# Optimization experiments

Hardware: AMD Instinct MI355X
Metric: run time of the kernel (lower is better)

Reference implementation:

```python
import jax, jax.numpy as jnp
import numpy as np

B, T, C = 4, 2048, 2048
H, D, L = 16, 128, 512


def _rope(x, cos, sin):
    # x: [B, T, H, D]; cos/sin: [T, D//2]; consecutive-pair complex rotation
    x2 = x.reshape(*x.shape[:-1], -1, 2)
    x0, x1 = x2[..., 0], x2[..., 1]
    c = cos[None, :, None, :]
    s = sin[None, :, None, :]
    o0 = x0 * c - x1 * s
    o1 = x0 * s + x1 * c
    return jnp.stack([o0, o1], axis=-1).reshape(x.shape)


def setup_inputs() -> dict:
    key = jax.random.key(0)
    ks = jax.random.split(key, 8)
    x = jax.random.normal(ks[0], (B, T, C), dtype=jnp.float32)
    # rotary table, theta = 10000
    inv_freq = 1.0 / (10000.0 ** (np.arange(0, D, 2, dtype=np.float32) / D))
    ang = np.outer(np.arange(T, dtype=np.float32), inv_freq)
    freqs_cos = jnp.asarray(np.cos(ang), dtype=jnp.float32)
    freqs_sin = jnp.asarray(np.sin(ang), dtype=jnp.float32)
    sc = 0.02
    wq = sc * jax.random.normal(ks[1], (H * D, C), dtype=jnp.float32)
    wkv_down = sc * jax.random.normal(ks[2], (L, C), dtype=jnp.float32)
    wk_up = sc * jax.random.normal(ks[3], (D, L), dtype=jnp.float32)
    wv_up = sc * jax.random.normal(ks[4], (D, L), dtype=jnp.float32)
    wo = sc * jax.random.normal(ks[5], (C, H * D), dtype=jnp.float32)
    return {"x": x, "freqs_cos": freqs_cos, "freqs_sin": freqs_sin,
            "wq": wq, "wkv_down": wkv_down, "wk_up": wk_up,
            "wv_up": wv_up, "wo": wo}


def reference(x, freqs_cos, freqs_sin, wq, wkv_down, wk_up, wv_up, wo):
    Bc, Tc, Cc = x.shape
    # query projection -> [B, T, H, D]
    q = jnp.einsum('btc,ec->bte', x, wq).reshape(Bc, Tc, H, D)
    # shared latent KV: [B, T, L]
    kv_latent = jnp.einsum('btc,lc->btl', x, wkv_down)
    # up-project to single shared head: [B, T, D]
    k = jnp.einsum('btl,dl->btd', kv_latent, wk_up)
    v = jnp.einsum('btl,dl->btd', kv_latent, wv_up)
    # RoPE on q (per head) and k (single shared head)
    q = _rope(q, freqs_cos, freqs_sin)
    k = _rope(k[:, :, None, :], freqs_cos, freqs_sin)[:, :, 0, :]
    # causal SDPA; k/v are shared across heads (MLA) so avoid expanding them
    scale = 1.0 / jnp.sqrt(jnp.asarray(D, dtype=x.dtype))
    scores = jnp.einsum('bthd,bsd->bhts', q, k) * scale  # [B, H, T, S]
    causal = jnp.tril(jnp.ones((Tc, Tc), dtype=bool))
    scores = jnp.where(causal[None, None, :, :], scores, jnp.finfo(x.dtype).min)
    probs = jax.nn.softmax(scores, axis=-1)
    y = jnp.einsum('bhts,bsd->bthd', probs, v).reshape(Bc, Tc, H * D)
    return jnp.einsum('bte,ce->btc', y, wo)
```

## Files before the change

### kernel.cpp

```cpp
#include <hip/hip_runtime.h>
#include <hip/hip_bf16.h>
#include <cstddef>

#define BB 4
#define TT 2048
#define CC 2048
#define HH 16
#define DD 128
#define LL 512

typedef _Float16 f16;
typedef f16 f16x2 __attribute__((ext_vector_type(2)));
typedef f16 f16x4 __attribute__((ext_vector_type(4)));
typedef f16 f16x8 __attribute__((ext_vector_type(8)));
typedef float f32x4 __attribute__((ext_vector_type(4)));

__device__ __forceinline__ void async_load16(void* lptr, const void* gptr) {
  __builtin_amdgcn_global_load_lds(
      (const __attribute__((address_space(1))) unsigned int*)gptr,
      (__attribute__((address_space(3))) unsigned int*)lptr, 16, 0, 0);
}

__global__ __launch_bounds__(512, 2) void mla_gemm_256(
    const f16* __restrict__ A, const f16* __restrict__ B,
    float* __restrict__ C, int M, int N, int K) {
  __shared__ __align__(16) f16 smem[2][2][256 * 64];

  const int tid = threadIdx.x;
  const int lane = tid & 63;
  const int w = tid >> 6;
  const int lnm = lane & 15, quad = lane >> 4;
  const int wm = w >> 2, wn = w & 3;

  const int nwg = gridDim.x;
  const int bid0 = blockIdx.x;
  const int q8 = nwg >> 3, r8 = nwg & 7;
  const int xcd = bid0 & 7, lid = bid0 >> 3;
  const int wg =
      (xcd < r8 ? xcd * (q8 + 1) : r8 * (q8 + 1) + (xcd - r8) * q8) + lid;
  const int ntc = N >> 8;
  const int m0 = (wg / ntc) * 256;
  const int n0 = (wg % ntc) * 256;

  const int srow = tid >> 3;
  const int sch = (tid & 7) ^ ((tid >> 3) & 7);
  const f16* Ag = A + (size_t)(m0 + srow) * K + sch * 8;
  const f16* Bg = B + (size_t)(n0 + srow) * K + sch * 8;

  auto stage = [&](int bi, int k0, int h) {
    const int mat = h >> 1;
    const int rb = (h & 1) * 128;
    const f16* g = (mat ? Bg : Ag) + (size_t)rb * K + k0;
    f16* l = &smem[bi][mat][rb * 64 + tid * 8];
    async_load16(l, g);
    async_load16(l + 4096, g + (size_t)64 * K);
  };

  const int rx8 = lnm & 7;
  auto rdA = [&](const f16* Ab, int i, int ks) -> f16x8 {
    return *(const f16x8*)&Ab[(wm * 128 + i * 16 + lnm) * 64 +
                              (((ks * 4 + quad) ^ rx8) * 8)];
  };
  auto rdB = [&](const f16* Bb, int j, int ks) -> f16x8 {
    return *(const f16x8*)&Bb[(wn * 64 + j * 16 + lnm) * 64 +
                              (((ks * 4 + quad) ^ rx8) * 8)];
  };

  f32x4 acc[8][4] = {};

  const int NT = K >> 6;

  stage(0, 0, 0);
  stage(0, 0, 1);
  stage(0, 0, 2);
  stage(0, 0, 3);
  stage(1, 64, 0);
  asm volatile("s_waitcnt vmcnt(2)" ::: "memory");
  __builtin_amdgcn_s_barrier();

  for (int t = 0; t < NT; ++t) {
    const int bi = t & 1;
    const f16* Ab = smem[bi][0];
    const f16* Bb = smem[bi][1];
    const int k1 = (t + 1 < NT ? t + 1 : t) << 6;
    const int k2 = (t + 2 < NT ? t + 2 : t) << 6;

    f16x8 Ar[4][2], Br[2][2];

#pragma unroll
    for (int i = 0; i < 4; i++)
#pragma unroll
      for (int ks = 0; ks < 2; ks++) Ar[i][ks] = rdA(Ab, i, ks);
#pragma unroll
    for (int j = 0; j < 2; j++)
#pragma unroll
      for (int ks = 0; ks < 2; ks++) Br[j][ks] = rdB(Bb, j, ks);
    stage(bi ^ 1, k1, 1);
    __builtin_amdgcn_s_barrier();
    asm volatile("s_waitcnt lgkmcnt(0)" ::: "memory");
    __builtin_amdgcn_s_setprio(1);
#pragma unroll
    for (int i = 0; i < 4; i++)
#pragma unroll
      for (int j = 0; j < 2; j++)
#pragma unroll
        for (int ks = 0; ks < 2; ks++)
          acc[i][j] = __builtin_amdgcn_mfma_f32_16x16x32_f16(
              Ar[i][ks], Br[j][ks], acc[i][j], 0, 0, 0);
    __builtin_amdgcn_s_setprio(0);
    __builtin_amdgcn_s_barrier();

#pragma unroll
    for (int j = 0; j < 2; j++)
#pragma unroll
      for (int ks = 0; ks < 2; ks++) Br[j][ks] = rdB(Bb, 2 + j, ks);
    stage(bi ^ 1, k1, 2);
    __builtin_amdgcn_s_barrier();
    asm volatile("s_waitcnt lgkmcnt(0)" ::: "memory");
    __builtin_amdgcn_s_setprio(1);
#pragma unroll
    for (int i = 0; i < 4; i++)
#pragma unroll
      for (int j = 0; j < 2; j++)
#pragma unroll
        for (int ks = 0; ks < 2; ks++)
          acc[i][2 + j] = __builtin_amdgcn_mfma_f32_16x16x32_f16(
              Ar[i][ks], Br[j][ks], acc[i][2 + j], 0, 0, 0);
    __builtin_amdgcn_s_setprio(0);
    __builtin_amdgcn_s_barrier();

#pragma unroll
    for (int i = 0; i < 4; i++)
#pragma unroll
      for (int ks = 0; ks < 2; ks++) Ar[i][ks] = rdA(Ab, 4 + i, ks);
    stage(bi ^ 1, k1, 3);
    __builtin_amdgcn_s_barrier();
    asm volatile("s_waitcnt lgkmcnt(0)" ::: "memory");
    __builtin_amdgcn_s_setprio(1);
#pragma unroll
    for (int i = 0; i < 4; i++)
#pragma unroll
      for (int j = 0; j < 2; j++)
#pragma unroll
        for (int ks = 0; ks < 2; ks++)
          acc[4 + i][2 + j] = __builtin_amdgcn_mfma_f32_16x16x32_f16(
              Ar[i][ks], Br[j][ks], acc[4 + i][2 + j], 0, 0, 0);
    __builtin_amdgcn_s_setprio(0);
    __builtin_amdgcn_s_barrier();

#pragma unroll
    for (int j = 0; j < 2; j++)
#pragma unroll
      for (int ks = 0; ks < 2; ks++) Br[j][ks] = rdB(Bb, j, ks);
    stage(bi, k2, 0);
    __builtin_amdgcn_s_barrier();
    asm volatile("s_waitcnt lgkmcnt(0)" ::: "memory");
    __builtin_amdgcn_s_setprio(1);
#pragma unroll
    for (int i = 0; i < 4; i++)
#pragma unroll
      for (int j = 0; j < 2; j++)
#pragma unroll
        for (int ks = 0; ks < 2; ks++)
          acc[4 + i][j] = __builtin_amdgcn_mfma_f32_16x16x32_f16(
              Ar[i][ks], Br[j][ks], acc[4 + i][j], 0, 0, 0);
    __builtin_amdgcn_s_setprio(0);
    asm volatile("s_waitcnt vmcnt(2)" ::: "memory");
    __builtin_amdgcn_s_barrier();
  }

  asm volatile("s_waitcnt vmcnt(0)" ::: "memory");

#pragma unroll
  for (int i = 0; i < 8; i++)
#pragma unroll
    for (int r = 0; r < 4; r++) {
      float* crow = C + (size_t)(m0 + wm * 128 + i * 16 + quad * 4 + r) * N +
                    n0 + wn * 64 + lnm;
#pragma unroll
      for (int j = 0; j < 4; j++) crow[j * 16] = acc[i][j][r];
    }
}

__global__ __launch_bounds__(256) void mla_gemm_mfma(
    const f16* __restrict__ A, const f16* __restrict__ B,
    float* __restrict__ C, int M, int N, int K) {
  __shared__ f16 As[128 * 32];
  __shared__ f16 Bs[128 * 32];

  const int tid = threadIdx.x;
  const int lane = tid & 63;
  const int w = tid >> 6;
  const int lnm = lane & 15, quad = lane >> 4;
  const int wm = w >> 1, wn = w & 1;
  const int m0 = blockIdx.y * 128;
  const int n0 = blockIdx.x * 128;

  const int srow = tid >> 2;
  const int skoff = (tid & 3) * 8;

  f32x4 acc[4][4] = {};

  for (int k0 = 0; k0 < K; k0 += 32) {
    const f16* ag = A + (size_t)(m0 + srow) * K + k0 + skoff;
    const f16* bg = B + (size_t)(n0 + srow) * K + k0 + skoff;
    async_load16(&As[(size_t)tid * 8], ag);
    async_load16(&As[(size_t)(256 + tid) * 8], ag + (size_t)64 * K);
    async_load16(&Bs[(size_t)tid * 8], bg);
    async_load16(&Bs[(size_t)(256 + tid) * 8], bg + (size_t)64 * K);
    __syncthreads();

    f16x8 af[4], bf[4];
#pragma unroll
    for (int i = 0; i < 4; i++)
      af[i] = *(const f16x8*)&As[(wm * 64 + i * 16 + lnm) * 32 + quad * 8];
#pragma unroll
    for (int j = 0; j < 4; j++)
      bf[j] = *(const f16x8*)&Bs[(wn * 64 + j * 16 + lnm) * 32 + quad * 8];
#pragma unroll
    for (int i = 0; i < 4; i++)
#pragma unroll
      for (int j = 0; j < 4; j++)
        acc[i][j] = __builtin_amdgcn_mfma_f32_16x16x32_f16(af[i], bf[j],
                                                           acc[i][j], 0, 0, 0);
    __syncthreads();
  }

#pragma unroll
  for (int i = 0; i < 4; i++)
#pragma unroll
    for (int r = 0; r < 4; r++) {
      float* crow = C + (size_t)(m0 + wm * 64 + i * 16 + quad * 4 + r) * N +
                    n0 + wn * 64 + lnm;
#pragma unroll
      for (int j = 0; j < 4; j++) crow[j * 16] = acc[i][j][r];
    }
}

__global__ __launch_bounds__(256) void mla_cvt_f16(
    const float4* __restrict__ in, f16* __restrict__ out, int n4) {
  int i = blockIdx.x * 256 + threadIdx.x;
  if (i >= n4) return;
  float4 v = in[i];
  f16x4 r = {(f16)v.x, (f16)v.y, (f16)v.z, (f16)v.w};
  *(f16x4*)(out + (size_t)i * 4) = r;
}

__global__ __launch_bounds__(256) void mla_rope_cvt(
    const float2* __restrict__ x, f16* __restrict__ o,
    const float* __restrict__ cosb, const float* __restrict__ sinb,
    int Hh, float scale, int total) {
  int idx = blockIdx.x * blockDim.x + threadIdx.x;
  if (idx >= total) return;
  const int Dh = DD / 2;
  int i = idx % Dh;
  int t = (idx / (Dh * Hh)) % TT;
  float c = cosb[t * Dh + i];
  float s = sinb[t * Dh + i];
  float2 v = x[idx];
  f16x2 r;
  r.x = (f16)((v.x * c - v.y * s) * scale);
  r.y = (f16)((v.x * s + v.y * c) * scale);
  *(f16x2*)(o + (size_t)idx * 2) = r;
}

__global__ __launch_bounds__(256) void mla_transpose_v(
    const float* __restrict__ v, f16* __restrict__ vt) {
  __shared__ float tl[32][33];
  const int b = blockIdx.z;
  const int t0 = blockIdx.x * 32;
  const int d0 = blockIdx.y * 32;
  const int tx = threadIdx.x & 31;
  const int ty = threadIdx.x >> 5;
#pragma unroll
  for (int k = 0; k < 4; k++)
    tl[ty + 8 * k][tx] = v[((size_t)(b * TT + t0 + ty + 8 * k)) * DD + d0 + tx];
  __syncthreads();
#pragma unroll
  for (int k = 0; k < 4; k++)
    vt[((size_t)(b * DD + d0 + ty + 8 * k)) * TT + t0 + tx] =
        (f16)tl[tx][ty + 8 * k];
}

__global__ __launch_bounds__(256, 2) void mla_flash2(
    const f16* __restrict__ qh, const f16* __restrict__ kh,
    const f16* __restrict__ vth, f16* __restrict__ y) {
  __shared__ f16 Ks[64 * 128];
  __shared__ f16 Vs[128 * 64];

  const int tid = threadIdx.x;
  const int lane = tid & 63;
  const int w = tid >> 6;
  const int lnm = lane & 15, quad = lane >> 4;

  const int bid = blockIdx.x;
  const int qt = (TT / 128 - 1) - (bid >> 6);
  const int bh = bid & 63;
  const int b = bh >> 4, h = bh & 15;
  const int q0b = qt * 128;
  const int q0 = q0b + w * 32;

  f16x8 qf[2][4];
#pragma unroll
  for (int qnb = 0; qnb < 2; qnb++) {
    const f16* qrow =
        qh + ((size_t)(b * TT + q0 + qnb * 16 + lnm) * HH + h) * DD;
#pragma unroll
    for (int c = 0; c < 4; c++)
      qf[qnb][c] = *(const f16x8*)(qrow + c * 32 + quad * 8);
  }

  f32x4 O[2][8] = {};
  float l_acc[2] = {0.f, 0.f};

  const int nst = (q0b + 128) / 64;
  const int wmax = q0 + 31;
  const f16* kbase = kh + (size_t)b * TT * DD;
  const f16* vbase = vth + (size_t)b * DD * TT;

  const int ks_row = tid >> 4;
  const int ks_col = ((tid & 15) ^ (tid >> 4)) * 8;
  const int vs_row = tid >> 3;
  const int vs_col = ((tid & 7) ^ ((tid >> 3) & 7)) * 8;

  for (int st = 0; st < nst; st++) {
    const int s0 = st * 64;
#pragma unroll
    for (int i = 0; i < 4; i++)
      async_load16(&Ks[(size_t)(i * 256 + tid) * 8],
                   kbase + (size_t)(s0 + i * 16 + ks_row) * DD + ks_col);
#pragma unroll
    for (int i = 0; i < 4; i++)
      async_load16(&Vs[(size_t)(i * 256 + tid) * 8],
                   vbase + (size_t)(i * 32 + vs_row) * TT + s0 + vs_col);
    __syncthreads();

    if (s0 <= wmax) {
      f32x4 S[2][4] = {};
#pragma unroll
      for (int sb = 0; sb < 4; sb++) {
        const int sl = sb * 16 + lnm;
#pragma unroll
        for (int c = 0; c < 4; c++) {
          f16x8 ka =
              *(const f16x8*)&Ks[sl * 128 + ((c * 4 + quad) ^ lnm) * 8];
          S[0][sb] = __builtin_amdgcn_mfma_f32_16x16x32_f16(ka, qf[0][c],
                                                            S[0][sb], 0, 0, 0);
          S[1][sb] = __builtin_amdgcn_mfma_f32_16x16x32_f16(ka, qf[1][c],
                                                            S[1][sb], 0, 0, 0);
        }
      }

      f16x4 P[2][4];
      const bool domask = (s0 + 63 > q0);
#pragma unroll
      for (int qnb = 0; qnb < 2; qnb++) {
        const int m_abs = q0 + qnb * 16 + lnm;
        float lp = 0.f;
#pragma unroll
        for (int sb = 0; sb < 4; sb++) {
          const int srow = s0 + sb * 16 + quad * 4;
          f16x4 ph;
#pragma unroll
          for (int j = 0; j < 4; j++) {
            float p = __expf(S[qnb][sb][j]);
            if (domask && (srow + j > m_abs)) p = 0.f;
            lp += p;
            ph[j] = (f16)p;
          }
          P[qnb][sb] = ph;
        }
        l_acc[qnb] += lp;
      }

#pragma unroll
      for (int sb = 0; sb < 4; sb++) {
        const int chb = sb * 2 + (quad >> 1);
        const int soff = (quad & 1) * 4;
#pragma unroll
        for (int db = 0; db < 8; db++) {
          const int d = db * 16 + lnm;
          f16x4 vb =
              *(const f16x4*)&Vs[d * 64 + ((chb ^ (d & 7)) * 8) + soff];
          O[0][db] = __builtin_amdgcn_mfma_f32_16x16x16f16(P[0][sb], vb,
                                                           O[0][db], 0, 0, 0);
          O[1][db] = __builtin_amdgcn_mfma_f32_16x16x16f16(P[1][sb], vb,
                                                           O[1][db], 0, 0, 0);
        }
      }
    }
    __syncthreads();
  }

#pragma unroll
  for (int qnb = 0; qnb < 2; qnb++) {
    float l = l_acc[qnb];
    l += __shfl_xor(l, 16, 64);
    l += __shfl_xor(l, 32, 64);
    l_acc[qnb] = l;
  }

#pragma unroll
  for (int qnb = 0; qnb < 2; qnb++) {
    float linv[4];
#pragma unroll
    for (int r = 0; r < 4; r++)
      linv[r] = 1.f / __shfl(l_acc[qnb], quad * 4 + r, 64);
#pragma unroll
    for (int db = 0; db < 8; db++)
#pragma unroll
      for (int r = 0; r < 4; r++) {
        size_t off =
            ((size_t)(b * TT + q0 + qnb * 16 + quad * 4 + r) * HH + h) * DD +
            db * 16 + lnm;
        y[off] = (f16)(O[qnb][db][r] * linv[r]);
      }
  }
}

extern "C" void kernel_launch(void* const* d_in, const int* in_sizes, int n_in,
                              void* d_out, int out_size, void* d_ws,
                              size_t ws_size, hipStream_t stream) {
  const float* x      = (const float*)d_in[0];
  const float* fcos   = (const float*)d_in[1];
  const float* fsin   = (const float*)d_in[2];
  const float* wq     = (const float*)d_in[3];
  const float* wdown  = (const float*)d_in[4];
  const float* wk_up  = (const float*)d_in[5];
  const float* wv_up  = (const float*)d_in[6];
  const float* wo     = (const float*)d_in[7];
  float* out = (float*)d_out;

  const int M = BB * TT;

  float* ws = (float*)d_ws;
  float* q      = ws;
  float* kv     = q + (size_t)M * CC;
  float* kk     = kv + (size_t)M * LL;
  float* vv     = kk + (size_t)M * DD;
  f16*   xh     = (f16*)(vv + (size_t)M * DD);
  f16*   wqh    = xh + (size_t)M * CC;
  f16*   wdownh = wqh + (size_t)CC * CC;
  f16*   wkuph  = wdownh + (size_t)LL * CC;
  f16*   wvuph  = wkuph + (size_t)DD * LL;
  f16*   woh    = wvuph + (size_t)DD * LL;
  f16*   kvh    = woh + (size_t)CC * CC;
  f16*   khb    = kvh + (size_t)M * LL;
  f16*   vth    = khb + (size_t)M * DD;
  f16*   qh     = xh;
  f16*   yh     = (f16*)q;

  dim3 blk(256);

  mla_cvt_f16<<<(M * CC / 4 + 255) / 256, blk, 0, stream>>>(
      (const float4*)x, xh, M * CC / 4);
  mla_cvt_f16<<<(CC * CC / 4 + 255) / 256, blk, 0, stream>>>(
      (const float4*)wq, wqh, CC * CC / 4);
  mla_cvt_f16<<<(LL * CC / 4 + 255) / 256, blk, 0, stream>>>(
      (const float4*)wdown, wdownh, LL * CC / 4);
  mla_cvt_f16<<<(DD * LL / 4 + 255) / 256, blk, 0, stream>>>(
      (const float4*)wk_up, wkuph, DD * LL / 4);
  mla_cvt_f16<<<(DD * LL / 4 + 255) / 256, blk, 0, stream>>>(
      (const float4*)wv_up, wvuph, DD * LL / 4);
  mla_cvt_f16<<<(CC * CC / 4 + 255) / 256, blk, 0, stream>>>(
      (const float4*)wo, woh, CC * CC / 4);

  mla_gemm_256<<<dim3((M / 256) * (CC / 256)), dim3(512), 0, stream>>>(
      xh, wqh, q, M, CC, CC);
  mla_gemm_mfma<<<dim3(LL / 128, M / 128), blk, 0, stream>>>(
      xh, wdownh, kv, M, LL, CC);

  mla_cvt_f16<<<(M * LL / 4 + 255) / 256, blk, 0, stream>>>(
      (const float4*)kv, kvh, M * LL / 4);
  mla_gemm_mfma<<<dim3(DD / 128, M / 128), blk, 0, stream>>>(
      kvh, wkuph, kk, M, DD, LL);
  mla_gemm_mfma<<<dim3(DD / 128, M / 128), blk, 0, stream>>>(
      kvh, wvuph, vv, M, DD, LL);

  {
    const float SCL = 0.08838834764831845f;
    int total_q = BB * TT * HH * (DD / 2);
    mla_rope_cvt<<<(total_q + 255) / 256, blk, 0, stream>>>(
        (const float2*)q, qh, fcos, fsin, HH, SCL, total_q);
    int total_k = BB * TT * (DD / 2);
    mla_rope_cvt<<<(total_k + 255) / 256, blk, 0, stream>>>(
        (const float2*)kk, khb, fcos, fsin, 1, 1.0f, total_k);
  }

  mla_transpose_v<<<dim3(TT / 32, DD / 32, BB), blk, 0, stream>>>(vv, vth);

  mla_flash2<<<dim3(BB * HH * (TT / 128)), blk, 0, stream>>>(qh, khb, vth, yh);

  mla_gemm_256<<<dim3((M / 256) * (CC / 256)), dim3(512), 0, stream>>>(
      yh, woh, out, M, CC, CC);
}
```

Measured before the change: 485.2 us.

## Fuse Q RoPE into GEMM epilogue and double-buffer flash attention K/V

The Q projection GEMM gains a templated epilogue that applies RoPE and the softmax scale, then writes fp16 directly. This removes the fp32 Q write and the separate rope/convert pass over the largest activation. The flash attention kernel double-buffers its K/V LDS tiles so the next tile's async loads overlap compute, and it switches the PV product to 16x16x32 MFMA with setprio hints. Costs are doubled LDS per block, which may reduce occupancy, and scattered per-element fp16 stores with cos/sin gathers in the epilogue. The workspace layout changes so qh and yh no longer alias xh.

```diff
diff --git a/kernel.cpp b/kernel.cpp
--- a/kernel.cpp
+++ b/kernel.cpp
@@ -21,9 +21,11 @@
       (__attribute__((address_space(3))) unsigned int*)lptr, 16, 0, 0);
 }
 
+template <int EPI>
 __global__ __launch_bounds__(512, 2) void mla_gemm_256(
     const f16* __restrict__ A, const f16* __restrict__ B,
-    float* __restrict__ C, int M, int N, int K) {
+    void* __restrict__ Cv, int M, int N, int K,
+    const float* __restrict__ cosb, const float* __restrict__ sinb) {
   __shared__ __align__(16) f16 smem[2][2][256 * 64];
 
   const int tid = threadIdx.x;
@@ -171,15 +173,40 @@
 
   asm volatile("s_waitcnt vmcnt(0)" ::: "memory");
 
-#pragma unroll
-  for (int i = 0; i < 8; i++)
-#pragma unroll
-    for (int r = 0; r < 4; r++) {
-      float* crow = C + (size_t)(m0 + wm * 128 + i * 16 + quad * 4 + r) * N +
-                    n0 + wn * 64 + lnm;
-#pragma unroll
-      for (int j = 0; j < 4; j++) crow[j * 16] = acc[i][j][r];
-    }
+  if constexpr (EPI == 0) {
+    float* C = (float*)Cv;
+#pragma unroll
+    for (int i = 0; i < 8; i++)
+#pragma unroll
+      for (int r = 0; r < 4; r++) {
+        float* crow = C + (size_t)(m0 + wm * 128 + i * 16 + quad * 4 + r) * N +
+                      n0 + wn * 64 + lnm;
+#pragma unroll
+        for (int j = 0; j < 4; j++) crow[j * 16] = acc[i][j][r];
+      }
+  } else {
+    f16* C = (f16*)Cv;
+    const float SCL = 0.08838834764831845f;
+#pragma unroll
+    for (int i = 0; i < 8; i++)
+#pragma unroll
+      for (int r = 0; r < 4; r++) {
+        const int m = m0 + wm * 128 + i * 16 + quad * 4 + r;
+        const int t = m & (TT - 1);
+#pragma unroll
+        for (int j = 0; j < 4; j++) {
+          const int col = n0 + wn * 64 + j * 16 + lnm;
+          float v = acc[i][j][r];
+          float u = __shfl_xor(v, 1, 64);
+          const int fi = (col & (DD - 1)) >> 1;
+          const float ct = cosb[t * (DD / 2) + fi];
+          const float st2 = sinb[t * (DD / 2) + fi];
+          const float o =
+              (lnm & 1) ? (u * st2 + v * ct) : (v * ct - u * st2);
+          C[(size_t)m * N + col] = (f16)(o * SCL);
+        }
+      }
+  }
 }
 
 __global__ __launch_bounds__(256) void mla_gemm_mfma(
@@ -285,8 +312,8 @@
 __global__ __launch_bounds__(256, 2) void mla_flash2(
     const f16* __restrict__ qh, const f16* __restrict__ kh,
     const f16* __restrict__ vth, f16* __restrict__ y) {
-  __shared__ f16 Ks[64 * 128];
-  __shared__ f16 Vs[128 * 64];
+  __shared__ f16 Ks[2][64 * 128];
+  __shared__ f16 Vs[2][128 * 64];
 
   const int tid = threadIdx.x;
   const int lane = tid & 63;
@@ -323,35 +350,48 @@
   const int vs_row = tid >> 3;
   const int vs_col = ((tid & 7) ^ ((tid >> 3) & 7)) * 8;
 
+  auto stage = [&](int buf, int st) {
+    const int s0 = st * 64;
+#pragma unroll
+    for (int i = 0; i < 4; i++)
+      async_load16(&Ks[buf][(size_t)(i * 256 + tid) * 8],
+                   kbase + (size_t)(s0 + i * 16 + ks_row) * DD + ks_col);
+#pragma unroll
+    for (int i = 0; i < 4; i++)
+      async_load16(&Vs[buf][(size_t)(i * 256 + tid) * 8],
+                   vbase + (size_t)(i * 32 + vs_row) * TT + s0 + vs_col);
+  };
+
+  stage(0, 0);
+  __syncthreads();
+
   for (int st = 0; st < nst; st++) {
+    const int cur = st & 1;
     const int s0 = st * 64;
-#pragma unroll
-    for (int i = 0; i < 4; i++)
-      async_load16(&Ks[(size_t)(i * 256 + tid) * 8],
-                   kbase + (size_t)(s0 + i * 16 + ks_row) * DD + ks_col);
-#pragma unroll
-    for (int i = 0; i < 4; i++)
-      async_load16(&Vs[(size_t)(i * 256 + tid) * 8],
-                   vbase + (size_t)(i * 32 + vs_row) * TT + s0 + vs_col);
-    __syncthreads();
+    if (st + 1 < nst) stage(cur ^ 1, st + 1);
 
     if (s0 <= wmax) {
+      const f16* Kc = Ks[cur];
+      const f16* Vc = Vs[cur];
+
       f32x4 S[2][4] = {};
+      __builtin_amdgcn_s_setprio(1);
 #pragma unroll
       for (int sb = 0; sb < 4; sb++) {
         const int sl = sb * 16 + lnm;
 #pragma unroll
         for (int c = 0; c < 4; c++) {
           f16x8 ka =
-              *(const f16x8*)&Ks[sl * 128 + ((c * 4 + quad) ^ lnm) * 8];
+              *(const f16x8*)&Kc[sl * 128 + ((c * 4 + quad) ^ lnm) * 8];
           S[0][sb] = __builtin_amdgcn_mfma_f32_16x16x32_f16(ka, qf[0][c],
                                                             S[0][sb], 0, 0, 0);
           S[1][sb] = __builtin_amdgcn_mfma_f32_16x16x32_f16(ka, qf[1][c],
                                                             S[1][sb], 0, 0, 0);
         }
       }
-
-      f16x4 P[2][4];
+      __builtin_amdgcn_s_setprio(0);
+
+      f16x8 P8[2][2];
       const bool domask = (s0 + 63 > q0);
 #pragma unroll
       for (int qnb = 0; qnb < 2; qnb++) {
@@ -360,34 +400,42 @@
 #pragma unroll
         for (int sb = 0; sb < 4; sb++) {
           const int srow = s0 + sb * 16 + quad * 4;
-          f16x4 ph;
 #pragma unroll
           for (int j = 0; j < 4; j++) {
             float p = __expf(S[qnb][sb][j]);
             if (domask && (srow + j > m_abs)) p = 0.f;
             lp += p;
-            ph[j] = (f16)p;
+            P8[qnb][sb >> 1][(sb & 1) * 4 + j] = (f16)p;
           }
-          P[qnb][sb] = ph;
         }
         l_acc[qnb] += lp;
       }
 
-#pragma unroll
-      for (int sb = 0; sb < 4; sb++) {
-        const int chb = sb * 2 + (quad >> 1);
+      __builtin_amdgcn_s_setprio(1);
+#pragma unroll
+      for (int c = 0; c < 2; c++) {
+        const int chlo = c * 4 + (quad >> 1);
         const int soff = (quad & 1) * 4;
 #pragma unroll
         for (int db = 0; db < 8; db++) {
           const int d = db * 16 + lnm;
-          f16x4 vb =
-              *(const f16x4*)&Vs[d * 64 + ((chb ^ (d & 7)) * 8) + soff];
-          O[0][db] = __builtin_amdgcn_mfma_f32_16x16x16f16(P[0][sb], vb,
-                                                           O[0][db], 0, 0, 0);
-          O[1][db] = __builtin_amdgcn_mfma_f32_16x16x16f16(P[1][sb], vb,
-                                                           O[1][db], 0, 0, 0);
+          const f16* vrow = &Vc[d * 64];
+          f16x4 vlo = *(const f16x4*)&vrow[((chlo ^ (d & 7)) * 8) + soff];
+          f16x4 vhi =
+              *(const f16x4*)&vrow[(((chlo + 2) ^ (d & 7)) * 8) + soff];
+          f16x8 vb;
+#pragma unroll
+          for (int j = 0; j < 4; j++) {
+            vb[j] = vlo[j];
+            vb[4 + j] = vhi[j];
+          }
+          O[0][db] = __builtin_amdgcn_mfma_f32_16x16x32_f16(P8[0][c], vb,
+                                                            O[0][db], 0, 0, 0);
+          O[1][db] = __builtin_amdgcn_mfma_f32_16x16x32_f16(P8[1][c], vb,
+                                                            O[1][db], 0, 0, 0);
         }
       }
+      __builtin_amdgcn_s_setprio(0);
     }
     __syncthreads();
   }
@@ -425,7 +473,7 @@
   const float* fcos   = (const float*)d_in[1];
   const float* fsin   = (const float*)d_in[2];
   const float* wq     = (const float*)d_in[3];
-  const float* wdown  = (const float*)d_in[4];
+  const float* wkv_dn = (const float*)d_in[4];
   const float* wk_up  = (const float*)d_in[5];
   const float* wv_up  = (const float*)d_in[6];
   const float* wo     = (const float*)d_in[7];
@@ -434,8 +482,8 @@
   const int M = BB * TT;
 
   float* ws = (float*)d_ws;
-  float* q      = ws;
-  float* kv     = q + (size_t)M * CC;
+  float* qbuf   = ws;
+  float* kv     = qbuf + (size_t)M * CC;
   float* kk     = kv + (size_t)M * LL;
   float* vv     = kk + (size_t)M * DD;
   f16*   xh     = (f16*)(vv + (size_t)M * DD);
@@ -447,8 +495,8 @@
   f16*   kvh    = woh + (size_t)CC * CC;
   f16*   khb    = kvh + (size_t)M * LL;
   f16*   vth    = khb + (size_t)M * DD;
-  f16*   qh     = xh;
-  f16*   yh     = (f16*)q;
+  f16*   qh     = (f16*)qbuf;
+  f16*   yh     = qh + (size_t)M * CC;
 
   dim3 blk(256);
 
@@ -457,7 +505,7 @@
   mla_cvt_f16<<<(CC * CC / 4 + 255) / 256, blk, 0, stream>>>(
       (const float4*)wq, wqh, CC * CC / 4);
   mla_cvt_f16<<<(LL * CC / 4 + 255) / 256, blk, 0, stream>>>(
-      (const float4*)wdown, wdownh, LL * CC / 4);
+      (const float4*)wkv_dn, wdownh, LL * CC / 4);
   mla_cvt_f16<<<(DD * LL / 4 + 255) / 256, blk, 0, stream>>>(
       (const float4*)wk_up, wkuph, DD * LL / 4);
   mla_cvt_f16<<<(DD * LL / 4 + 255) / 256, blk, 0, stream>>>(
@@ -465,8 +513,8 @@
   mla_cvt_f16<<<(CC * CC / 4 + 255) / 256, blk, 0, stream>>>(
       (const float4*)wo, woh, CC * CC / 4);
 
-  mla_gemm_256<<<dim3((M / 256) * (CC / 256)), dim3(512), 0, stream>>>(
-      xh, wqh, q, M, CC, CC);
+  mla_gemm_256<1><<<dim3((M / 256) * (CC / 256)), dim3(512), 0, stream>>>(
+      xh, wqh, qh, M, CC, CC, fcos, fsin);
   mla_gemm_mfma<<<dim3(LL / 128, M / 128), blk, 0, stream>>>(
       xh, wdownh, kv, M, LL, CC);
 
@@ -478,10 +526,6 @@
       kvh, wvuph, vv, M, DD, LL);
 
   {
-    const float SCL = 0.08838834764831845f;
-    int total_q = BB * TT * HH * (DD / 2);
-    mla_rope_cvt<<<(total_q + 255) / 256, blk, 0, stream>>>(
-        (const float2*)q, qh, fcos, fsin, HH, SCL, total_q);
     int total_k = BB * TT * (DD / 2);
     mla_rope_cvt<<<(total_k + 255) / 256, blk, 0, stream>>>(
         (const float2*)kk, khb, fcos, fsin, 1, 1.0f, total_k);
@@ -491,6 +535,6 @@
 
   mla_flash2<<<dim3(BB * HH * (TT / 128)), blk, 0, stream>>>(qh, khb, vth, yh);
 
-  mla_gemm_256<<<dim3((M / 256) * (CC / 256)), dim3(512), 0, stream>>>(
-      yh, woh, out, M, CC, CC);
-}
+  mla_gemm_256<0><<<dim3((M / 256) * (CC / 256)), dim3(512), 0, stream>>>(
+      yh, woh, out, M, CC, CC, nullptr, nullptr);
+}
```

Result: faster. 469.7 us (-3.2%).
